# Kernel optimization log

Measured on AMD Instinct MI355X. Metric: run time of the kernel, lower is better.

Reference implementation:

```python
import jax, jax.numpy as jnp
import numpy as np

# Fixed per-step coefficients from the module __init__ (K = 16 steps)
_H = jnp.array([-0.73437643, 3.319645, 2.1290164, 3.6901689, 3.302721, 3.2154958,
                2.9151256, 3.1718695, 3.1084518, 2.6179547, 2.235003, 1.2864777,
                0.52327204, -0.08344932, -1.8249638, 3.0859442], dtype=jnp.float32)
_D = jnp.array([3.3848417, -0.07072583, 3.691287, 3.3074934, 3.2120926, 2.9196491,
                3.1727686, 3.1054153, 2.621943, 2.2355895, 1.2878408, 0.52468026,
                0.12632068, 0.14482783, 0.3153498, 0.13054803], dtype=jnp.float32)
_T = jnp.array([3.1538513, -1.0211663, 1.3714716, 1.0718397, 1.0049332, 0.68078244,
                1.0151638, 0.8858697, 0.4037103, 0.01490025, -0.90781677, -1.6859558,
                -1.9241625, -2.0441303, 0.279356, 0.1315174], dtype=jnp.float32)


@jax.custom_vjp
def spike(v_scaled):
    # Heaviside forward with surrogate gradient (matches SpikeFunction)
    return (v_scaled > 0).astype(v_scaled.dtype)

def _spike_fwd(v_scaled):
    return spike(v_scaled), v_scaled

def _spike_bwd(v_scaled, g):
    surrogate = jnp.maximum(1.0 - jnp.abs(v_scaled), 0.0)
    return (g * surrogate,)

spike.defvjp(_spike_fwd, _spike_bwd)


def setup_inputs() -> dict:
    key = jax.random.key(0)
    x = jax.random.normal(key, (16, 4096, 1024), dtype=jnp.float32)
    return {"x": x}


def reference(x) -> jnp.ndarray:
    zeros = jnp.zeros_like(x)

    def step(carry, hdt):
        v, z, out = carry
        h_t, d_t, T_t = hdt
        v = v - z * h_t
        v_scaled = (v - T_t) / (jnp.abs(v) + 1.0)
        z = spike(v_scaled)
        out = out + z * d_t
        return (v, z, out), None

    (_, _, out), _ = jax.lax.scan(step, (x, zeros, zeros), (_H, _D, _T))
    return out
```

## Files before the change

### kernel.cpp

```cpp
#include <hip/hip_runtime.h>


typedef float f32x4 __attribute__((ext_vector_type(4)));

__device__ __constant__ const float kH[16] = {
    -0.73437643f, 3.319645f,   2.1290164f,  3.6901689f,
    3.302721f,    3.2154958f,  2.9151256f,  3.1718695f,
    3.1084518f,   2.6179547f,  2.235003f,   1.2864777f,
    0.52327204f, -0.08344932f, -1.8249638f, 3.0859442f};

__device__ __constant__ const float kD[16] = {
    3.3848417f, -0.07072583f, 3.691287f,   3.3074934f,
    3.2120926f,  2.9196491f,  3.1727686f,  3.1054153f,
    2.621943f,   2.2355895f,  1.2878408f,  0.52468026f,
    0.12632068f, 0.14482783f, 0.3153498f,  0.13054803f};

__device__ __constant__ const float kT[16] = {
    3.1538513f, -1.0211663f,  1.3714716f,  1.0718397f,
    1.0049332f,  0.68078244f, 1.0151638f,  0.8858697f,
    0.4037103f,  0.01490025f, -0.90781677f, -1.6859558f,
    -1.9241625f, -2.0441303f, 0.279356f,   0.1315174f};

__device__ __forceinline__ f32x4 splat4(float s) {
    f32x4 r = {s, s, s, s};
    return r;
}

__device__ __forceinline__ f32x4 spike4(f32x4 v) {
    f32x4 zn = splat4(0.0f);
    f32x4 o  = splat4(0.0f);
#pragma unroll
    for (int t = 0; t < 16; ++t) {
        v = __builtin_elementwise_fma(zn, splat4(kH[t]), v);
        zn.x = (v.x > kT[t]) ? -1.0f : 0.0f;
        zn.y = (v.y > kT[t]) ? -1.0f : 0.0f;
        zn.z = (v.z > kT[t]) ? -1.0f : 0.0f;
        zn.w = (v.w > kT[t]) ? -1.0f : 0.0f;
        o = __builtin_elementwise_fma(zn, splat4(-kD[t]), o);
    }
    return o;
}

__global__ __launch_bounds__(256) void spike_kernel(const f32x4* __restrict__ x,
                                                    f32x4* __restrict__ out,
                                                    int n4) {
    const int T = gridDim.x * blockDim.x;
    int i = blockIdx.x * blockDim.x + threadIdx.x;

    for (; i + 7 * T < n4; i += 8 * T) {
        f32x4 a0 = x[i];
        f32x4 a1 = x[i + T];
        f32x4 a2 = x[i + 2 * T];
        f32x4 a3 = x[i + 3 * T];
        f32x4 a4 = x[i + 4 * T];
        f32x4 a5 = x[i + 5 * T];
        f32x4 a6 = x[i + 6 * T];
        f32x4 a7 = x[i + 7 * T];
        f32x4 r0 = spike4(a0);
        f32x4 r1 = spike4(a1);
        f32x4 r2 = spike4(a2);
        f32x4 r3 = spike4(a3);
        f32x4 r4 = spike4(a4);
        f32x4 r5 = spike4(a5);
        f32x4 r6 = spike4(a6);
        f32x4 r7 = spike4(a7);
        __builtin_nontemporal_store(r0, &out[i]);
        __builtin_nontemporal_store(r1, &out[i + T]);
        __builtin_nontemporal_store(r2, &out[i + 2 * T]);
        __builtin_nontemporal_store(r3, &out[i + 3 * T]);
        __builtin_nontemporal_store(r4, &out[i + 4 * T]);
        __builtin_nontemporal_store(r5, &out[i + 5 * T]);
        __builtin_nontemporal_store(r6, &out[i + 6 * T]);
        __builtin_nontemporal_store(r7, &out[i + 7 * T]);
    }
    for (; i < n4; i += T) {
        f32x4 r = spike4(x[i]);
        __builtin_nontemporal_store(r, &out[i]);
    }
}

extern "C" void kernel_launch(void* const* d_in, const int* in_sizes, int n_in,
                              void* d_out, int out_size, void* d_ws, size_t ws_size,
                              hipStream_t stream) {
    const float* x = (const float*)d_in[0];
    float* out = (float*)d_out;
    int n = in_sizes[0];
    int n4 = n >> 2;

    const int block = 256;
    int grid = (n4 + 8 * block - 1) / (8 * block);

    spike_kernel<<<grid, block, 0, stream>>>(
        (const f32x4*)x, (f32x4*)out, n4);
}
```

Measured before the change: 100.1 us.

## Software-pipeline loads with double-buffered register groups in persistent-style kernel

Replaces the grid-stride kernel with a templated kernel in which each thread processes a fixed number of 4-vector groups. The next group's loads are issued before computing and storing the current group, so memory latency overlaps with the 16-step spike arithmetic. A fallback generic kernel with a capped grid handles sizes that don't divide evenly. The new kernel uses fewer, longer-lived blocks, which may reduce memory parallelism or raise register pressure.

```diff
diff --git a/kernel.cpp b/kernel.cpp
--- a/kernel.cpp
+++ b/kernel.cpp
@@ -41,37 +41,57 @@
     return o;
 }
 
-__global__ __launch_bounds__(256) void spike_kernel(const f32x4* __restrict__ x,
-                                                    f32x4* __restrict__ out,
-                                                    int n4) {
+template <int NIT>
+__global__ __launch_bounds__(256, 4) void spike_pipe(const f32x4* __restrict__ x,
+                                                     f32x4* __restrict__ out) {
+    const int T = gridDim.x * blockDim.x;
+    const int t = blockIdx.x * blockDim.x + threadIdx.x;
+    const int G = 4 * T;
+
+    f32x4 A0 = x[t], A1 = x[t + T], A2 = x[t + 2 * T], A3 = x[t + 3 * T];
+    f32x4 B0, B1, B2, B3;
+
+#pragma unroll
+    for (int g = 0; g < NIT; g += 2) {
+        if (g + 1 < NIT) {
+            const int b = t + (g + 1) * G;
+            B0 = x[b]; B1 = x[b + T]; B2 = x[b + 2 * T]; B3 = x[b + 3 * T];
+        }
+        {
+            const int a = t + g * G;
+            __builtin_nontemporal_store(spike4(A0), &out[a]);
+            __builtin_nontemporal_store(spike4(A1), &out[a + T]);
+            __builtin_nontemporal_store(spike4(A2), &out[a + 2 * T]);
+            __builtin_nontemporal_store(spike4(A3), &out[a + 3 * T]);
+        }
+        if (g + 2 < NIT) {
+            const int a = t + (g + 2) * G;
+            A0 = x[a]; A1 = x[a + T]; A2 = x[a + 2 * T]; A3 = x[a + 3 * T];
+        }
+        if (g + 1 < NIT) {
+            const int b = t + (g + 1) * G;
+            __builtin_nontemporal_store(spike4(B0), &out[b]);
+            __builtin_nontemporal_store(spike4(B1), &out[b + T]);
+            __builtin_nontemporal_store(spike4(B2), &out[b + 2 * T]);
+            __builtin_nontemporal_store(spike4(B3), &out[b + 3 * T]);
+        }
+    }
+}
+
+__global__ __launch_bounds__(256) void spike_generic(const f32x4* __restrict__ x,
+                                                     f32x4* __restrict__ out,
+                                                     int n4) {
     const int T = gridDim.x * blockDim.x;
     int i = blockIdx.x * blockDim.x + threadIdx.x;
-
-    for (; i + 7 * T < n4; i += 8 * T) {
-        f32x4 a0 = x[i];
-        f32x4 a1 = x[i + T];
-        f32x4 a2 = x[i + 2 * T];
-        f32x4 a3 = x[i + 3 * T];
-        f32x4 a4 = x[i + 4 * T];
-        f32x4 a5 = x[i + 5 * T];
-        f32x4 a6 = x[i + 6 * T];
-        f32x4 a7 = x[i + 7 * T];
-        f32x4 r0 = spike4(a0);
-        f32x4 r1 = spike4(a1);
-        f32x4 r2 = spike4(a2);
-        f32x4 r3 = spike4(a3);
-        f32x4 r4 = spike4(a4);
-        f32x4 r5 = spike4(a5);
-        f32x4 r6 = spike4(a6);
-        f32x4 r7 = spike4(a7);
+    for (; i + 3 * T < n4; i += 4 * T) {
+        f32x4 r0 = spike4(x[i]);
+        f32x4 r1 = spike4(x[i + T]);
+        f32x4 r2 = spike4(x[i + 2 * T]);
+        f32x4 r3 = spike4(x[i + 3 * T]);
         __builtin_nontemporal_store(r0, &out[i]);
         __builtin_nontemporal_store(r1, &out[i + T]);
         __builtin_nontemporal_store(r2, &out[i + 2 * T]);
         __builtin_nontemporal_store(r3, &out[i + 3 * T]);
-        __builtin_nontemporal_store(r4, &out[i + 4 * T]);
-        __builtin_nontemporal_store(r5, &out[i + 5 * T]);
-        __builtin_nontemporal_store(r6, &out[i + 6 * T]);
-        __builtin_nontemporal_store(r7, &out[i + 7 * T]);
     }
     for (; i < n4; i += T) {
         f32x4 r = spike4(x[i]);
@@ -88,8 +108,17 @@
     int n4 = n >> 2;
 
     const int block = 256;
-    int grid = (n4 + 8 * block - 1) / (8 * block);
+    constexpr int NIT = 8;
+    const int per_thread = 4 * NIT;
 
-    spike_kernel<<<grid, block, 0, stream>>>(
-        (const f32x4*)x, (f32x4*)out, n4);
+    if (n4 % (block * per_thread) == 0) {
+        int grid = n4 / (block * per_thread);
+        spike_pipe<NIT><<<grid, block, 0, stream>>>(
+            (const f32x4*)x, (f32x4*)out);
+    } else {
+        int grid = (n4 + 4 * block - 1) / (4 * block);
+        if (grid > 2048) grid = 2048;
+        spike_generic<<<grid, block, 0, stream>>>(
+            (const f32x4*)x, (f32x4*)out, n4);
+    }
 }
```

After: 105.1 us. 5.0% more time.
